# Optimization experiments

Hardware: AMD Instinct MI355X
Metric: run time of the kernel (lower is better)

The kernel has to match this reference:

```python
import jax, jax.numpy as jnp
import numpy as np

WH, WW = 16, 16            # window size
NUM_HEADS = 8


def _relative_position_index(wh, ww):
    ch = jnp.arange(wh)
    cw = jnp.arange(ww)
    coords = jnp.stack(jnp.meshgrid(ch, cw, indexing='ij'))        # [2, wh, ww]
    coords = coords.reshape(2, -1)                                  # [2, N]
    rel = coords[:, :, None] - coords[:, None, :]                   # [2, N, N]
    rel = rel.transpose(1, 2, 0)                                    # [N, N, 2]
    idx = (rel[..., 0] + wh - 1) * (2 * ww - 1) + (rel[..., 1] + ww - 1)
    return idx                                                      # [N, N] int32


def setup_inputs() -> dict:
    key = jax.random.key(0)
    ks = jax.random.split(key, 7)
    B, N, C = 128, WH * WW, 512
    x = jax.random.normal(ks[0], (B, N, C), dtype=jnp.float32)
    y = jax.random.normal(ks[1], (B, N, C), dtype=jnp.float32)
    # Linear weights stored as [in, out]; init ~ standard scale
    q_w = jax.random.normal(ks[2], (C, C), dtype=jnp.float32) * (C ** -0.5)
    kv_w = jax.random.normal(ks[3], (C, 2 * C), dtype=jnp.float32) * (C ** -0.5)
    proj_w = jax.random.normal(ks[4], (C, C), dtype=jnp.float32) * (C ** -0.5)
    proj_b = jax.random.normal(ks[5], (C,), dtype=jnp.float32) * 0.01
    n_rel = (2 * WH - 1) * (2 * WW - 1)  # 961
    bias_table = jax.random.normal(ks[6], (n_rel, NUM_HEADS), dtype=jnp.float32) * 0.02
    return {"x": x, "y": y, "q_w": q_w, "kv_w": kv_w,
            "proj_w": proj_w, "proj_b": proj_b, "bias_table": bias_table}


def reference(x, y, q_w, kv_w, proj_w, proj_b, bias_table):
    B, N1, C = x.shape
    _, N2, _ = y.shape
    H = NUM_HEADS
    d = C // H
    scale = d ** -0.5

    q = (x @ q_w).reshape(B, N1, H, d).transpose(0, 2, 1, 3)        # [B,H,N1,d]
    kv = (y @ kv_w).reshape(B, N2, 2, H, d)
    k = kv[:, :, 0].transpose(0, 2, 1, 3)                           # [B,H,N2,d]
    v = kv[:, :, 1].transpose(0, 2, 1, 3)                           # [B,H,N2,d]

    attn = jnp.einsum('bhqd,bhkd->bhqk', q, k) * scale              # [B,H,N1,N2]

    idx = _relative_position_index(WH, WW)                          # [N, N]
    rel_bias = bias_table[idx.reshape(-1)].reshape(N1, N2, H)       # gather
    rel_bias = rel_bias.transpose(2, 0, 1)                          # [H,N1,N2]
    attn = attn + rel_bias[None]

    attn = jax.nn.softmax(attn, axis=-1)
    out = jnp.einsum('bhqk,bhkd->bhqd', attn, v)                    # [B,H,N1,d]
    out = out.transpose(0, 2, 1, 3).reshape(B, N1, C)
    out = out @ proj_w + proj_b
    return out
```

## Files before the change

kernel.cpp:

```cpp
#include <hip/hip_runtime.h>

typedef unsigned short u16;
typedef __attribute__((ext_vector_type(8))) short short8;
typedef __attribute__((ext_vector_type(4))) float floatx4;

__device__ __forceinline__ float bf2f(u16 v){
  union { unsigned int u; float f; } x; x.u = ((unsigned int)v) << 16; return x.f;
}
__device__ __forceinline__ u16 f2bf(float f){
  union { float f; unsigned int u; } x; x.f = f;
  unsigned int r = x.u + 0x7FFFu + ((x.u >> 16) & 1u);
  return (u16)(r >> 16);
}

__device__ __forceinline__ void async16(const void* g, void* l){
  __builtin_amdgcn_global_load_lds(
      (__attribute__((address_space(1))) unsigned int*)const_cast<void*>(g),
      (__attribute__((address_space(3))) unsigned int*)l, 16, 0, 0);
}

__global__ void transpose_f32(const float* __restrict__ in, u16* __restrict__ out,
                              int R, int C){
  __shared__ u16 t[32][33];
  const int tx = threadIdx.x;
  const int c0 = blockIdx.x * 32, r0 = blockIdx.y * 32;
  for (int i = tx; i < 1024; i += 256){
    int r = i >> 5, c = i & 31;
    t[r][c] = f2bf(in[(size_t)(r0 + r) * C + c0 + c]);
  }
  __syncthreads();
  for (int i = tx; i < 1024; i += 256){
    int r = i >> 5, c = i & 31;
    out[(size_t)(c0 + r) * R + r0 + c] = t[c][r];
  }
}

__global__ void bias_expand(const float* __restrict__ table, u16* __restrict__ Bm){
  int i = blockIdx.x * 256 + threadIdx.x;
  int q = i >> 8, k = i & 255;
  int rh = (q >> 4) - (k >> 4) + 15;
  int rw = (q & 15) - (k & 15) + 15;
  int idx = rh * 31 + rw;
  #pragma unroll
  for (int h = 0; h < 8; h++) Bm[h * 65536 + i] = f2bf(table[(size_t)idx * 8 + h]);
}

template<int MODE, bool A_FP32>
__global__ __launch_bounds__(256)
void gemm_bt(const void* __restrict__ A, const u16* __restrict__ Bt,
             void* __restrict__ O0, u16* __restrict__ O1,
             const float* __restrict__ bias)
{
  __shared__ __align__(16) u16 As[128 * 64];
  __shared__ __align__(16) u16 Bs[128 * 64];
  const int tid  = threadIdx.x;
  const int lane = tid & 63, wave = tid >> 6;
  const int q16  = lane & 15, quad = lane >> 4;
  const int wr   = wave >> 1, wc = wave & 1;
  const int rowBase = blockIdx.y * 128;
  const int colBase = blockIdx.x * 128;

  const u16*   Ab16 = (const u16*)A   + (size_t)rowBase * 512;
  const float* Af32 = (const float*)A + (size_t)rowBase * 512;
  const u16*   Bw   = Bt + (size_t)colBase * 512;

  floatx4 acc[4][4];
  #pragma unroll
  for (int i = 0; i < 4; i++)
    #pragma unroll
    for (int j = 0; j < 4; j++) acc[i][j] = floatx4{0.f, 0.f, 0.f, 0.f};

  int sr[4], sc[4];
  #pragma unroll
  for (int j = 0; j < 4; j++){
    int p = tid + j * 256;
    sr[j] = p >> 3;
    sc[j] = ((p & 7) ^ (sr[j] & 7)) * 8;
  }

  for (int kt = 0; kt < 8; kt++){
    __syncthreads();
    if (A_FP32){
      #pragma unroll
      for (int j = 0; j < 4; j++){
        const float* src = Af32 + (size_t)sr[j] * 512 + kt * 64 + sc[j];
        float4 f0 = ((const float4*)src)[0];
        float4 f1 = ((const float4*)src)[1];
        short8 v;
        v[0] = (short)f2bf(f0.x); v[1] = (short)f2bf(f0.y);
        v[2] = (short)f2bf(f0.z); v[3] = (short)f2bf(f0.w);
        v[4] = (short)f2bf(f1.x); v[5] = (short)f2bf(f1.y);
        v[6] = (short)f2bf(f1.z); v[7] = (short)f2bf(f1.w);
        *(short8*)(As + (size_t)(tid + j * 256) * 8) = v;
      }
    } else {
      #pragma unroll
      for (int j = 0; j < 4; j++){
        u16* dA = As + (size_t)(j * 256 + wave * 64) * 8;
        async16(Ab16 + (size_t)sr[j] * 512 + kt * 64 + sc[j], dA);
      }
    }
    #pragma unroll
    for (int j = 0; j < 4; j++){
      u16* dB = Bs + (size_t)(j * 256 + wave * 64) * 8;
      async16(Bw + (size_t)sr[j] * 512 + kt * 64 + sc[j], dB);
    }
    __syncthreads();
    #pragma unroll
    for (int kk = 0; kk < 2; kk++){
      short8 af[4], bfr[4];
      #pragma unroll
      for (int mt = 0; mt < 4; mt++){
        int r  = wr * 64 + mt * 16 + q16;
        int ph = ((kk * 4 + quad) ^ (r & 7)) * 8;
        af[mt] = *(const short8*)(As + r * 64 + ph);
      }
      #pragma unroll
      for (int nt = 0; nt < 4; nt++){
        int r  = wc * 64 + nt * 16 + q16;
        int ph = ((kk * 4 + quad) ^ (r & 7)) * 8;
        bfr[nt] = *(const short8*)(Bs + r * 64 + ph);
      }
      #pragma unroll
      for (int mt = 0; mt < 4; mt++)
        #pragma unroll
        for (int nt = 0; nt < 4; nt++)
          acc[mt][nt] = __builtin_amdgcn_mfma_f32_16x16x32_bf16(
              af[mt], bfr[nt], acc[mt][nt], 0, 0, 0);
    }
  }

  #pragma unroll
  for (int mt = 0; mt < 4; mt++){
    #pragma unroll
    for (int nt = 0; nt < 4; nt++){
      const floatx4 v = acc[mt][nt];
      const int col = colBase + wc * 64 + nt * 16 + q16;
      #pragma unroll
      for (int r = 0; r < 4; r++){
        const int row = rowBase + wr * 64 + mt * 16 + quad * 4 + r;
        if (MODE == 0){
          int bb = row >> 8, n = row & 255, hh = col >> 6, dd = col & 63;
          ((u16*)O0)[(((size_t)(bb * 8 + hh)) * 256 + n) * 64 + dd] = f2bf(v[r]);
        } else if (MODE == 1){
          int bb = row >> 8, key = row & 255;
          int two = col >> 9, hh = (col >> 6) & 7, dd = col & 63;
          if (two == 0)
            ((u16*)O0)[(((size_t)(bb * 8 + hh)) * 256 + key) * 64 + dd] = f2bf(v[r]);
          else
            O1[(((size_t)(bb * 8 + hh)) * 64 + dd) * 256 + key] = f2bf(v[r]);
        } else {
          ((float*)O0)[(size_t)row * 512 + col] = v[r] + bias[col];
        }
      }
    }
  }
}

__global__ __launch_bounds__(256)
void attn_kernel(const u16* __restrict__ Qb, const u16* __restrict__ Kb,
                 const u16* __restrict__ Vtb, const u16* __restrict__ Bm,
                 u16* __restrict__ Ob)
{
  constexpr int PS = 264;
  __shared__ __align__(16) u16 Vs[64 * PS];
  __shared__ __align__(16) u16 Pss[4 * 16 * PS];
  const int bh = blockIdx.x;
  const int b = bh >> 3, h = bh & 7;
  const u16* Qp = Qb  + (size_t)bh * 256 * 64;
  const u16* Kp = Kb  + (size_t)bh * 256 * 64;
  const u16* Vp = Vtb + (size_t)bh * 64 * 256;
  const u16* Bp = Bm  + (size_t)h * 65536;
  const int tid = threadIdx.x;
  const int lane = tid & 63, wave = tid >> 6;
  const int q16 = lane & 15, quad = lane >> 4;
  u16* Pw = Pss + wave * 16 * PS;

  for (int i = tid; i < 64 * 32; i += 256){
    int dd = i >> 5, kc = (i & 31) * 8;
    *(short8*)(Vs + dd * PS + kc) = *(const short8*)(Vp + dd * 256 + kc);
  }
  __syncthreads();

  for (int chunk = 0; chunk < 4; chunk++){
    const int qbase = wave * 64 + chunk * 16;
    const short8 qa0 = *(const short8*)(Qp + (qbase + q16) * 64 + quad * 8);
    const short8 qa1 = *(const short8*)(Qp + (qbase + q16) * 64 + 32 + quad * 8);

    floatx4 acc[16];
    #pragma unroll
    for (int kt = 0; kt < 16; kt++) acc[kt] = floatx4{0.f, 0.f, 0.f, 0.f};
    #pragma unroll
    for (int kt = 0; kt < 16; kt++){
      const u16* kr = Kp + (kt * 16 + q16) * 64 + quad * 8;
      acc[kt] = __builtin_amdgcn_mfma_f32_16x16x32_bf16(
          qa0, *(const short8*)(kr), acc[kt], 0, 0, 0);
      acc[kt] = __builtin_amdgcn_mfma_f32_16x16x32_bf16(
          qa1, *(const short8*)(kr + 32), acc[kt], 0, 0, 0);
    }

    floatx4 mrow = {-3e38f, -3e38f, -3e38f, -3e38f};
    #pragma unroll
    for (int kt = 0; kt < 16; kt++){
      const u16* bb = Bp + (qbase + quad * 4) * 256 + kt * 16 + q16;
      floatx4 v = acc[kt];
      #pragma unroll
      for (int r = 0; r < 4; r++){
        float t = v[r] * 0.125f + bf2f(bb[(size_t)r * 256]);
        v[r] = t;
        mrow[r] = fmaxf(mrow[r], t);
      }
      acc[kt] = v;
    }
    #pragma unroll
    for (int off = 1; off < 16; off <<= 1){
      #pragma unroll
      for (int r = 0; r < 4; r++)
        mrow[r] = fmaxf(mrow[r], __shfl_xor(mrow[r], off, 64));
    }

    floatx4 lrow = {0.f, 0.f, 0.f, 0.f};
    #pragma unroll
    for (int kt = 0; kt < 16; kt++){
      floatx4 v = acc[kt];
      #pragma unroll
      for (int r = 0; r < 4; r++){
        float e = exp2f((v[r] - mrow[r]) * 1.4426950408889634f);
        v[r] = e;
        lrow[r] += e;
      }
      #pragma unroll
      for (int r = 0; r < 4; r++)
        Pw[(quad * 4 + r) * PS + kt * 16 + q16] = f2bf(v[r]);
    }
    #pragma unroll
    for (int off = 1; off < 16; off <<= 1){
      #pragma unroll
      for (int r = 0; r < 4; r++) lrow[r] += __shfl_xor(lrow[r], off, 64);
    }

    __syncthreads();

    short8 pa[8];
    #pragma unroll
    for (int k2 = 0; k2 < 8; k2++)
      pa[k2] = *(const short8*)(Pw + q16 * PS + k2 * 32 + quad * 8);
    floatx4 o[4];
    #pragma unroll
    for (int nt = 0; nt < 4; nt++) o[nt] = floatx4{0.f, 0.f, 0.f, 0.f};
    #pragma unroll
    for (int nt = 0; nt < 4; nt++)
      #pragma unroll
      for (int k2 = 0; k2 < 8; k2++){
        const short8 vb = *(const short8*)(Vs + (nt * 16 + q16) * PS + k2 * 32 + quad * 8);
        o[nt] = __builtin_amdgcn_mfma_f32_16x16x32_bf16(pa[k2], vb, o[nt], 0, 0, 0);
      }

    floatx4 rl;
    #pragma unroll
    for (int r = 0; r < 4; r++) rl[r] = 1.0f / lrow[r];
    #pragma unroll
    for (int nt = 0; nt < 4; nt++)
      #pragma unroll
      for (int r = 0; r < 4; r++){
        int q = qbase + quad * 4 + r;
        Ob[((size_t)(b * 256 + q)) * 512 + h * 64 + nt * 16 + q16] =
            f2bf(o[nt][r] * rl[r]);
      }
  }
}

extern "C" void kernel_launch(void* const* d_in, const int* in_sizes, int n_in,
                              void* d_out, int out_size, void* d_ws, size_t ws_size,
                              hipStream_t stream)
{
  (void)in_sizes; (void)n_in; (void)out_size; (void)ws_size;
  const float* x      = (const float*)d_in[0];
  const float* y      = (const float*)d_in[1];
  const float* q_w    = (const float*)d_in[2];
  const float* kv_w   = (const float*)d_in[3];
  const float* proj_w = (const float*)d_in[4];
  const float* proj_b = (const float*)d_in[5];
  const float* btab   = (const float*)d_in[6];
  float* out = (float*)d_out;
  char* w = (char*)d_ws;

  u16* Qb   = (u16*)(w);
  u16* Kb   = (u16*)(w + 33554432);
  u16* Vtb  = (u16*)(w + 67108864);
  u16* Ab   = (u16*)(w + 100663296);
  u16* qwT  = (u16*)(w + 134217728);
  u16* kvwT = (u16*)(w + 134742016);
  u16* pwT  = (u16*)(w + 135790592);
  u16* Bm   = (u16*)(w + 136314880);

  transpose_f32<<<dim3(16, 16), 256, 0, stream>>>(q_w,    qwT,  512, 512);
  transpose_f32<<<dim3(32, 16), 256, 0, stream>>>(kv_w,   kvwT, 512, 1024);
  transpose_f32<<<dim3(16, 16), 256, 0, stream>>>(proj_w, pwT,  512, 512);
  bias_expand<<<dim3(256), 256, 0, stream>>>(btab, Bm);

  gemm_bt<0, true ><<<dim3(4, 256), 256, 0, stream>>>(x,  qwT,  Qb,  nullptr, nullptr);
  gemm_bt<1, true ><<<dim3(8, 256), 256, 0, stream>>>(y,  kvwT, Kb,  Vtb,     nullptr);
  attn_kernel<<<dim3(1024), 256, 0, stream>>>(Qb, Kb, Vtb, Bm, Ab);
  gemm_bt<2, false><<<dim3(4, 256), 256, 0, stream>>>(Ab, pwT,  out, nullptr, proj_b);
}
```

Measured before the change: 447.5 us.

## Double-buffer GEMM LDS tiles and swizzle block order for L2 reuse

```diff
diff --git a/kernel.cpp b/kernel.cpp
--- a/kernel.cpp
+++ b/kernel.cpp
@@ -11,6 +11,14 @@
   union { float f; unsigned int u; } x; x.f = f;
   unsigned int r = x.u + 0x7FFFu + ((x.u >> 16) & 1u);
   return (u16)(r >> 16);
+}
+__device__ __forceinline__ short8 cvt8(float4 f0, float4 f1){
+  short8 v;
+  v[0] = (short)f2bf(f0.x); v[1] = (short)f2bf(f0.y);
+  v[2] = (short)f2bf(f0.z); v[3] = (short)f2bf(f0.w);
+  v[4] = (short)f2bf(f1.x); v[5] = (short)f2bf(f1.y);
+  v[6] = (short)f2bf(f1.z); v[7] = (short)f2bf(f1.w);
+  return v;
 }
 
 __device__ __forceinline__ void async16(const void* g, void* l){
@@ -51,14 +59,20 @@
              void* __restrict__ O0, u16* __restrict__ O1,
              const float* __restrict__ bias)
 {
-  __shared__ __align__(16) u16 As[128 * 64];
-  __shared__ __align__(16) u16 Bs[128 * 64];
+  __shared__ __align__(16) u16 As[2][128 * 64];
+  __shared__ __align__(16) u16 Bs[2][128 * 64];
   const int tid  = threadIdx.x;
   const int lane = tid & 63, wave = tid >> 6;
   const int q16  = lane & 15, quad = lane >> 4;
   const int wr   = wave >> 1, wc = wave & 1;
-  const int rowBase = blockIdx.y * 128;
-  const int colBase = blockIdx.x * 128;
+
+  constexpr int GX  = (MODE == 1) ? 8 : 4;
+  constexpr int LGX = (MODE == 1) ? 3 : 2;
+  constexpr int CPX = GX * 32;
+  const int bid = blockIdx.y * GX + blockIdx.x;
+  const int swz = (bid & 7) * CPX + (bid >> 3);
+  const int rowBase = (swz >> LGX) * 128;
+  const int colBase = (swz & (GX - 1)) * 128;
 
   const u16*   Ab16 = (const u16*)A   + (size_t)rowBase * 512;
   const float* Af32 = (const float*)A + (size_t)rowBase * 512;
@@ -78,34 +92,55 @@
     sc[j] = ((p & 7) ^ (sr[j] & 7)) * 8;
   }
 
+  if (A_FP32){
+    #pragma unroll
+    for (int j = 0; j < 4; j++){
+      const float* src = Af32 + (size_t)sr[j] * 512 + sc[j];
+      float4 f0 = ((const float4*)src)[0];
+      float4 f1 = ((const float4*)src)[1];
+      *(short8*)(&As[0][(size_t)(tid + j * 256) * 8]) = cvt8(f0, f1);
+    }
+  } else {
+    #pragma unroll
+    for (int j = 0; j < 4; j++){
+      u16* dA = &As[0][(size_t)(j * 256 + wave * 64) * 8];
+      async16(Ab16 + (size_t)sr[j] * 512 + sc[j], dA);
+    }
+  }
+  #pragma unroll
+  for (int j = 0; j < 4; j++){
+    u16* dB = &Bs[0][(size_t)(j * 256 + wave * 64) * 8];
+    async16(Bw + (size_t)sr[j] * 512 + sc[j], dB);
+  }
+  __syncthreads();
+
+  int cur = 0;
   for (int kt = 0; kt < 8; kt++){
-    __syncthreads();
-    if (A_FP32){
+    const int nb = cur ^ 1;
+
+    float4 f0[4], f1[4];
+    if (kt < 7){
+      if (A_FP32){
+        #pragma unroll
+        for (int j = 0; j < 4; j++){
+          const float* src = Af32 + (size_t)sr[j] * 512 + (kt + 1) * 64 + sc[j];
+          f0[j] = ((const float4*)src)[0];
+          f1[j] = ((const float4*)src)[1];
+        }
+      } else {
+        #pragma unroll
+        for (int j = 0; j < 4; j++){
+          u16* dA = &As[nb][(size_t)(j * 256 + wave * 64) * 8];
+          async16(Ab16 + (size_t)sr[j] * 512 + (kt + 1) * 64 + sc[j], dA);
+        }
+      }
       #pragma unroll
       for (int j = 0; j < 4; j++){
-        const float* src = Af32 + (size_t)sr[j] * 512 + kt * 64 + sc[j];
-        float4 f0 = ((const float4*)src)[0];
-        float4 f1 = ((const float4*)src)[1];
-        short8 v;
-        v[0] = (short)f2bf(f0.x); v[1] = (short)f2bf(f0.y);
-        v[2] = (short)f2bf(f0.z); v[3] = (short)f2bf(f0.w);
-        v[4] = (short)f2bf(f1.x); v[5] = (short)f2bf(f1.y);
-        v[6] = (short)f2bf(f1.z); v[7] = (short)f2bf(f1.w);
-        *(short8*)(As + (size_t)(tid + j * 256) * 8) = v;
-      }
-    } else {
-      #pragma unroll
-      for (int j = 0; j < 4; j++){
-        u16* dA = As + (size_t)(j * 256 + wave * 64) * 8;
-        async16(Ab16 + (size_t)sr[j] * 512 + kt * 64 + sc[j], dA);
-      }
-    }
-    #pragma unroll
-    for (int j = 0; j < 4; j++){
-      u16* dB = Bs + (size_t)(j * 256 + wave * 64) * 8;
-      async16(Bw + (size_t)sr[j] * 512 + kt * 64 + sc[j], dB);
-    }
-    __syncthreads();
+        u16* dB = &Bs[nb][(size_t)(j * 256 + wave * 64) * 8];
+        async16(Bw + (size_t)sr[j] * 512 + (kt + 1) * 64 + sc[j], dB);
+      }
+    }
+
     #pragma unroll
     for (int kk = 0; kk < 2; kk++){
       short8 af[4], bfr[4];
@@ -113,13 +148,13 @@
       for (int mt = 0; mt < 4; mt++){
         int r  = wr * 64 + mt * 16 + q16;
         int ph = ((kk * 4 + quad) ^ (r & 7)) * 8;
-        af[mt] = *(const short8*)(As + r * 64 + ph);
+        af[mt] = *(const short8*)(&As[cur][r * 64 + ph]);
       }
       #pragma unroll
       for (int nt = 0; nt < 4; nt++){
         int r  = wc * 64 + nt * 16 + q16;
         int ph = ((kk * 4 + quad) ^ (r & 7)) * 8;
-        bfr[nt] = *(const short8*)(Bs + r * 64 + ph);
+        bfr[nt] = *(const short8*)(&Bs[cur][r * 64 + ph]);
       }
       #pragma unroll
       for (int mt = 0; mt < 4; mt++)
@@ -128,6 +163,15 @@
           acc[mt][nt] = __builtin_amdgcn_mfma_f32_16x16x32_bf16(
               af[mt], bfr[nt], acc[mt][nt], 0, 0, 0);
     }
+
+    if (A_FP32 && kt < 7){
+      #pragma unroll
+      for (int j = 0; j < 4; j++)
+        *(short8*)(&As[nb][(size_t)(tid + j * 256) * 8]) = cvt8(f0[j], f1[j]);
+    }
+
+    __syncthreads();
+    cur = nb;
   }
 
   #pragma unroll
```

Result: no change. 441.8 us (-1.3%).

## Pre-convert inputs to bf16 and triple-buffer async GEMM loads with larger tiles

Applied to the files above, without the earlier changes.

```diff
diff --git a/kernel.cpp b/kernel.cpp
--- a/kernel.cpp
+++ b/kernel.cpp
@@ -12,11 +12,29 @@
   unsigned int r = x.u + 0x7FFFu + ((x.u >> 16) & 1u);
   return (u16)(r >> 16);
 }
+__device__ __forceinline__ short8 cvt8(float4 f0, float4 f1){
+  short8 v;
+  v[0] = (short)f2bf(f0.x); v[1] = (short)f2bf(f0.y);
+  v[2] = (short)f2bf(f0.z); v[3] = (short)f2bf(f0.w);
+  v[4] = (short)f2bf(f1.x); v[5] = (short)f2bf(f1.y);
+  v[6] = (short)f2bf(f1.z); v[7] = (short)f2bf(f1.w);
+  return v;
+}
 
 __device__ __forceinline__ void async16(const void* g, void* l){
   __builtin_amdgcn_global_load_lds(
       (__attribute__((address_space(1))) unsigned int*)const_cast<void*>(g),
       (__attribute__((address_space(3))) unsigned int*)l, 16, 0, 0);
+}
+
+__global__ __launch_bounds__(256)
+void conv_bf16(const float* __restrict__ in, u16* __restrict__ out, int n8){
+  const int stride = gridDim.x * 256;
+  for (int i = blockIdx.x * 256 + threadIdx.x; i < n8; i += stride){
+    float4 f0 = ((const float4*)in)[(size_t)i * 2];
+    float4 f1 = ((const float4*)in)[(size_t)i * 2 + 1];
+    *(short8*)(out + (size_t)i * 8) = cvt8(f0, f1);
+  }
 }
 
 __global__ void transpose_f32(const float* __restrict__ in, u16* __restrict__ out,
@@ -45,24 +63,28 @@
   for (int h = 0; h < 8; h++) Bm[h * 65536 + i] = f2bf(table[(size_t)idx * 8 + h]);
 }
 
-template<int MODE, bool A_FP32>
-__global__ __launch_bounds__(256)
-void gemm_bt(const void* __restrict__ A, const u16* __restrict__ Bt,
+template<int MODE, int GX>
+__global__ __launch_bounds__(512, 2)
+void gemm_bt(const u16* __restrict__ A, const u16* __restrict__ Bt,
              void* __restrict__ O0, u16* __restrict__ O1,
              const float* __restrict__ bias)
 {
-  __shared__ __align__(16) u16 As[128 * 64];
-  __shared__ __align__(16) u16 Bs[128 * 64];
+  __shared__ __align__(16) u16 As[3][256 * 64];
+  __shared__ __align__(16) u16 Bs[3][128 * 64];
   const int tid  = threadIdx.x;
   const int lane = tid & 63, wave = tid >> 6;
   const int q16  = lane & 15, quad = lane >> 4;
   const int wr   = wave >> 1, wc = wave & 1;
-  const int rowBase = blockIdx.y * 128;
-  const int colBase = blockIdx.x * 128;
-
-  const u16*   Ab16 = (const u16*)A   + (size_t)rowBase * 512;
-  const float* Af32 = (const float*)A + (size_t)rowBase * 512;
-  const u16*   Bw   = Bt + (size_t)colBase * 512;
+
+  constexpr int NWG = 128 * GX;
+  constexpr int CPX = NWG / 8;
+  const int bid = blockIdx.x;
+  const int swz = (bid & 7) * CPX + (bid >> 3);
+  const int rowBase = (swz / GX) * 256;
+  const int colBase = (swz % GX) * 128;
+
+  const u16* Ap = A  + (size_t)rowBase * 512;
+  const u16* Bp = Bt + (size_t)colBase * 512;
 
   floatx4 acc[4][4];
   #pragma unroll
@@ -70,42 +92,41 @@
     #pragma unroll
     for (int j = 0; j < 4; j++) acc[i][j] = floatx4{0.f, 0.f, 0.f, 0.f};
 
-  int sr[4], sc[4];
+  int sra[4], sca[4];
   #pragma unroll
   for (int j = 0; j < 4; j++){
-    int p = tid + j * 256;
-    sr[j] = p >> 3;
-    sc[j] = ((p & 7) ^ (sr[j] & 7)) * 8;
-  }
-
+    int p = tid + j * 512;
+    sra[j] = p >> 3;
+    sca[j] = ((p & 7) ^ (sra[j] & 7)) * 8;
+  }
+
+  auto STAGE = [&](int slot, int kt){
+    #pragma unroll
+    for (int j = 0; j < 4; j++){
+      u16* d = &As[slot][(size_t)(j * 512 + wave * 64) * 8];
+      async16(Ap + (size_t)sra[j] * 512 + kt * 64 + sca[j], d);
+    }
+    #pragma unroll
+    for (int j = 0; j < 2; j++){
+      u16* d = &Bs[slot][(size_t)(j * 512 + wave * 64) * 8];
+      async16(Bp + (size_t)sra[j] * 512 + kt * 64 + sca[j], d);
+    }
+  };
+
+  STAGE(0, 0);
+  STAGE(1, 1);
+
+  #pragma unroll
   for (int kt = 0; kt < 8; kt++){
-    __syncthreads();
-    if (A_FP32){
-      #pragma unroll
-      for (int j = 0; j < 4; j++){
-        const float* src = Af32 + (size_t)sr[j] * 512 + kt * 64 + sc[j];
-        float4 f0 = ((const float4*)src)[0];
-        float4 f1 = ((const float4*)src)[1];
-        short8 v;
-        v[0] = (short)f2bf(f0.x); v[1] = (short)f2bf(f0.y);
-        v[2] = (short)f2bf(f0.z); v[3] = (short)f2bf(f0.w);
-        v[4] = (short)f2bf(f1.x); v[5] = (short)f2bf(f1.y);
-        v[6] = (short)f2bf(f1.z); v[7] = (short)f2bf(f1.w);
-        *(short8*)(As + (size_t)(tid + j * 256) * 8) = v;
-      }
-    } else {
-      #pragma unroll
-      for (int j = 0; j < 4; j++){
-        u16* dA = As + (size_t)(j * 256 + wave * 64) * 8;
-        async16(Ab16 + (size_t)sr[j] * 512 + kt * 64 + sc[j], dA);
-      }
-    }
-    #pragma unroll
-    for (int j = 0; j < 4; j++){
-      u16* dB = Bs + (size_t)(j * 256 + wave * 64) * 8;
-      async16(Bw + (size_t)sr[j] * 512 + kt * 64 + sc[j], dB);
-    }
-    __syncthreads();
+    const int cs = kt % 3;
+    if (kt < 7) asm volatile("s_waitcnt vmcnt(6)" ::: "memory");
+    else        asm volatile("s_waitcnt vmcnt(0)" ::: "memory");
+    __builtin_amdgcn_s_barrier();
+    __builtin_amdgcn_sched_barrier(0);
+    if (kt + 2 < 8) STAGE((kt + 2) % 3, kt + 2);
+    __builtin_amdgcn_sched_barrier(0);
+
+    __builtin_amdgcn_s_setprio(1);
     #pragma unroll
     for (int kk = 0; kk < 2; kk++){
       short8 af[4], bfr[4];
@@ -113,13 +134,13 @@
       for (int mt = 0; mt < 4; mt++){
         int r  = wr * 64 + mt * 16 + q16;
         int ph = ((kk * 4 + quad) ^ (r & 7)) * 8;
-        af[mt] = *(const short8*)(As + r * 64 + ph);
+        af[mt] = *(const short8*)(&As[cs][r * 64 + ph]);
       }
       #pragma unroll
       for (int nt = 0; nt < 4; nt++){
         int r  = wc * 64 + nt * 16 + q16;
         int ph = ((kk * 4 + quad) ^ (r & 7)) * 8;
-        bfr[nt] = *(const short8*)(Bs + r * 64 + ph);
+        bfr[nt] = *(const short8*)(&Bs[cs][r * 64 + ph]);
       }
       #pragma unroll
       for (int mt = 0; mt < 4; mt++)
@@ -128,6 +149,7 @@
           acc[mt][nt] = __builtin_amdgcn_mfma_f32_16x16x32_bf16(
               af[mt], bfr[nt], acc[mt][nt], 0, 0, 0);
     }
+    __builtin_amdgcn_s_setprio(0);
   }
 
   #pragma unroll
@@ -299,8 +321,10 @@
   transpose_f32<<<dim3(16, 16), 256, 0, stream>>>(proj_w, pwT,  512, 512);
   bias_expand<<<dim3(256), 256, 0, stream>>>(btab, Bm);
 
-  gemm_bt<0, true ><<<dim3(4, 256), 256, 0, stream>>>(x,  qwT,  Qb,  nullptr, nullptr);
-  gemm_bt<1, true ><<<dim3(8, 256), 256, 0, stream>>>(y,  kvwT, Kb,  Vtb,     nullptr);
+  conv_bf16<<<dim3(2048), 256, 0, stream>>>(x, Ab, 2097152);
+  gemm_bt<0, 4><<<dim3(512),  512, 0, stream>>>(Ab, qwT,  Qb,  nullptr, nullptr);
+  conv_bf16<<<dim3(2048), 256, 0, stream>>>(y, Ab, 2097152);
+  gemm_bt<1, 8><<<dim3(1024), 512, 0, stream>>>(Ab, kvwT, Kb,  Vtb,     nullptr);
   attn_kernel<<<dim3(1024), 256, 0, stream>>>(Qb, Kb, Vtb, Bm, Ab);
-  gemm_bt<2, false><<<dim3(4, 256), 256, 0, stream>>>(Ab, pwT,  out, nullptr, proj_b);
-}
+  gemm_bt<2, 4><<<dim3(512),  512, 0, stream>>>(Ab, pwT,  out, nullptr, proj_b);
+}
```

Result: faster. 410.8 us (-8.2%).
